# Optimization experiments

Measured on AMD Instinct MI355X. Metric: run time of the kernel, lower is better.

## Reference

```python
import jax, jax.numpy as jnp
import numpy as np

N = 100000          # n_nodes
E = 1600000         # n_edges (avg degree 16)
IN = 256            # in_dim
OUT = 16            # out_dim
SLOPE = 0.2         # leaky_relu negative slope
DROP = 0.5          # dropout rate


def _xavier(key, shape):
    fan_in, fan_out = shape
    std = (2.0 / (fan_in + fan_out)) ** 0.5
    return std * jax.random.normal(key, shape, jnp.float32)


def setup_inputs() -> dict:
    key = jax.random.key(0)
    ks = jax.random.split(key, 10)
    x = jax.random.normal(ks[0], (N, IN), jnp.float32)
    row = jax.random.randint(ks[1], (E,), 0, N, jnp.int32)
    col = jax.random.randint(ks[2], (E,), 0, N, jnp.int32)
    edge_w = jax.random.uniform(ks[3], (E,), jnp.float32)
    W1 = _xavier(ks[4], (IN, IN // 2)); b1 = jnp.zeros((IN // 2,), jnp.float32)
    W2 = _xavier(ks[5], (IN // 2, IN // 4)); b2 = jnp.zeros((IN // 4,), jnp.float32)
    W3 = _xavier(ks[6], (IN // 4, IN // 8)); b3 = jnp.zeros((IN // 8,), jnp.float32)
    W4 = _xavier(ks[7], (IN // 8, OUT)); b4 = jnp.zeros((OUT,), jnp.float32)
    # dropout mask (training-mode dropout made deterministic; pre-scaled by 1/(1-p))
    drop_mask = (jax.random.uniform(ks[8], (N, IN // 2)) > DROP).astype(jnp.float32) / (1.0 - DROP)
    return dict(x=x, row=row, col=col, edge_w=edge_w,
                W1=W1, b1=b1, W2=W2, b2=b2, W3=W3, b3=b3, W4=W4, b4=b4,
                drop_mask=drop_mask)


def reference(x, row, col, edge_w, W1, b1, W2, b2, W3, b3, W4, b4, drop_mask):
    def spmm(h):
        # out[i] = sum over edges (i <- j): w_ij * h[j]   (sparse adj @ h)
        return jax.ops.segment_sum(edge_w[:, None] * h[col], row, num_segments=N)

    lrelu = lambda v: jax.nn.leaky_relu(v, SLOPE)

    h = spmm(x @ W1) + b1          # gc1: [N, IN/2]
    h = lrelu(h) * drop_mask       # leaky_relu + dropout
    h = spmm(h @ W2) + b2          # gc2: [N, IN/4]
    h = lrelu(h)
    h = lrelu(h @ W3 + b3)         # clf hidden: [N, IN/8]
    return h @ W4 + b4             # logits: [N, OUT]
```

## Files before the change

kernel.cpp:

```cpp
#include <hip/hip_runtime.h>
#include <hip/hip_bf16.h>

#define N_NODES 100000
#define N_EDGES 1600000
#define SLOPE_ 0.2f
#define NBK 196
#define BCAP 9216
#define NCB 13
#define KEYS (512 * NCB)
#define BINBLK2 1000
#define CHUNK2 1600
#define PREPW 20
#define PMBLK 1563

typedef __attribute__((ext_vector_type(8))) short bf16x8;
typedef __attribute__((ext_vector_type(4))) float f32x4;

__device__ __forceinline__ short f2bf(float f) {
    __hip_bfloat16 h = __float2bfloat16(f);
    return *reinterpret_cast<short*>(&h);
}
__device__ __forceinline__ float bflo(unsigned u) { return __uint_as_float(u << 16); }
__device__ __forceinline__ float bfhi(unsigned u) { return __uint_as_float(u & 0xFFFF0000u); }
__device__ __forceinline__ float bf2f(short s) {
    return __uint_as_float(((unsigned)(unsigned short)s) << 16);
}


__global__ void countA_k(const int* __restrict__ row, int* __restrict__ counts,
                         const float* __restrict__ W1, const float* __restrict__ W2,
                         const float* __restrict__ mask,
                         short* __restrict__ Bp1, short* __restrict__ Bp2,
                         unsigned* __restrict__ mp) {
    int t = threadIdx.x;
    if (blockIdx.x < BINBLK2) {
        __shared__ int hist[NBK];
        for (int i = t; i < NBK; i += 256) hist[i] = 0;
        __syncthreads();
        int e0 = blockIdx.x * CHUNK2;
        for (int i = t; i < CHUNK2; i += 256)
            atomicAdd(&hist[row[e0 + i] >> 9], 1);
        __syncthreads();
        for (int i = t; i < NBK; i += 256)
            counts[(size_t)i * BINBLK2 + blockIdx.x] = hist[i];
        return;
    }
    int bi = blockIdx.x - BINBLK2;
    if (bi < PREPW) {
        int i = bi * 256 + t;
        if (i < 4096) {
            int ln = i & 15, nt = (i >> 4) & 7, g = (i >> 7) & 3, ks = i >> 9;
            int n = nt * 16 + ln, k0 = ks * 32 + g * 8;
            bf16x8 v;
#pragma unroll
            for (int j = 0; j < 8; j++) v[j] = f2bf(W1[(k0 + j) * 128 + n]);
            *(bf16x8*)(Bp1 + (size_t)i * 8) = v;
        } else if (i < 5120) {
            int c = i - 4096;
            int ln = c & 15, nt = (c >> 4) & 3, g = (c >> 6) & 3, ks = c >> 8;
            int n = nt * 16 + ln, k0 = ks * 32 + g * 8;
            bf16x8 v;
#pragma unroll
            for (int j = 0; j < 8; j++) v[j] = f2bf(W2[(k0 + j) * 64 + n]);
            *(bf16x8*)(Bp2 + (size_t)c * 8) = v;
        }
        return;
    }
    int pb = bi - PREPW;
    long fbase = (long)pb * 8192;
    int wv = t >> 6, lane = t & 63;
    const long FLIM = (long)N_NODES * 128;
    for (int it = 0; it < 32; ++it) {
        long f = fbase + it * 256 + wv * 64 + lane;
        float v = (f < FLIM) ? mask[f] : 0.f;
        unsigned long long bl = __ballot(v != 0.f);
        if (lane == 0) {
            long w = f >> 5;
            if (w < (long)N_NODES * 4)
                *(unsigned long long*)(mp + w) = bl;
        }
    }
}


__global__ void scanA_k(const int* __restrict__ counts, int* __restrict__ bases,
                        int* __restrict__ cur) {
    __shared__ int s[256];
    int b = blockIdx.x, t = threadIdx.x;
    const int* src = counts + (size_t)b * BINBLK2;
    int v[4];
    int loc = 0;
#pragma unroll
    for (int j = 0; j < 4; j++) {
        int idx = t * 4 + j;
        v[j] = (idx < BINBLK2) ? src[idx] : 0;
        loc += v[j];
    }
    s[t] = loc;
    __syncthreads();
    for (int off = 1; off < 256; off <<= 1) {
        int u = (t >= off) ? s[t - off] : 0;
        __syncthreads();
        s[t] += u;
        __syncthreads();
    }
    int run = s[t] - loc;
    int* dst = bases + (size_t)b * BINBLK2;
#pragma unroll
    for (int j = 0; j < 4; j++) {
        int idx = t * 4 + j;
        if (idx < BINBLK2) dst[idx] = run;
        run += v[j];
    }
    if (t == 255) cur[b] = min(s[255], BCAP);
}


__global__ void scatterA_k(const int* __restrict__ row, const int* __restrict__ col,
                           const float* __restrict__ ew, const int* __restrict__ bases,
                           int2* __restrict__ binned) {
    __shared__ int off[NBK];
    int t = threadIdx.x, blk = blockIdx.x;
    for (int i = t; i < NBK; i += 256) off[i] = bases[(size_t)i * BINBLK2 + blk];
    __syncthreads();
    int e0 = blk * CHUNK2;
    for (int i = t; i < CHUNK2; i += 256) {
        int e = e0 + i;
        int r = row[e], c = col[e];
        int b = r >> 9;
        int p = atomicAdd(&off[b], 1);
        if (p < BCAP)
            binned[(size_t)b * BCAP + p] =
                make_int2(((r & 511) << 17) | c, __float_as_int(ew[e]));
    }
}


__global__ void __launch_bounds__(512) passB_k(const int2* __restrict__ binned,
                                               const int* __restrict__ cur,
                                               unsigned* __restrict__ cw,
                                               int* __restrict__ row_ptr) {
    __shared__ int hist[KEYS];
    __shared__ int offs[KEYS];
    __shared__ int ssum[512];
    __shared__ int bexc[256];
    int t = threadIdx.x, b = blockIdx.x;
    const int2* src = binned + (size_t)b * BCAP;
    int cnt = cur[b];
    if (cnt > BCAP) cnt = BCAP;

    if (t < 256) bexc[t] = (t < NBK) ? min(cur[t], BCAP) : 0;
    __syncthreads();
    for (int off2 = 1; off2 < 256; off2 <<= 1) {
        int v = (t < 256 && t >= off2) ? bexc[t - off2] : 0;
        __syncthreads();
        if (t < 256) bexc[t] += v;
        __syncthreads();
    }
    int gbase = bexc[b] - cnt;

    for (int i = t; i < KEYS; i += 512) hist[i] = 0;
    __syncthreads();

    for (int i = t; i < cnt; i += 512) {
        int2 v = src[i];
        int c = v.x & 0x1FFFF, lr = v.x >> 17;
        atomicAdd(&hist[lr * NCB + (c >> 13)], 1);
    }
    __syncthreads();

    int loc[NCB];
    int tot = 0;
#pragma unroll
    for (int j = 0; j < NCB; j++) {
        loc[j] = tot;
        tot += hist[t * NCB + j];
    }
    ssum[t] = tot;
    __syncthreads();
    for (int off2 = 1; off2 < 512; off2 <<= 1) {
        int v = (t >= off2) ? ssum[t - off2] : 0;
        __syncthreads();
        ssum[t] += v;
        __syncthreads();
    }
    int base = ssum[t] - tot;
#pragma unroll
    for (int j = 0; j < NCB; j++) offs[t * NCB + j] = base + loc[j];

    int grow = b * 512 + t;
    if (grow <= N_NODES) row_ptr[grow] = gbase + base;
    __syncthreads();

    for (int i = t; i < cnt; i += 512) {
        int2 v = src[i];
        int c = v.x & 0x1FFFF, lr = v.x >> 17;
        int p = gbase + atomicAdd(&offs[lr * NCB + (c >> 13)], 1);
        unsigned wb = (unsigned)(unsigned short)f2bf(__int_as_float(v.y));
        cw[p] = ((unsigned)c << 15) | (wb & 0x7FFFu);
    }
}


template <int K, int COLS, bool ABF16>
__global__ __launch_bounds__(512) void gemm_p(const void* __restrict__ Ap,
                                              const short* __restrict__ Bp,
                                              short* __restrict__ out, int M) {
    constexpr int NT = COLS / 16;
    constexpr int NKS = K / 32;
    __shared__ short Bs[K * COLS];
    int t = threadIdx.x;
    for (int i = t; i < K * COLS / 8; i += 512)
        *(bf16x8*)(Bs + (size_t)i * 8) = *(const bf16x8*)(Bp + (size_t)i * 8);
    __syncthreads();

    int l = t & 63, wv = t >> 6;
    int ln = l & 15, g = l >> 4;
    int row0 = blockIdx.x * 256 + wv * 32;
    int r0 = row0 + ln, r1 = row0 + 16 + ln;
    int cr0 = min(r0, M - 1), cr1 = min(r1, M - 1);

    f32x4 acc[2][NT];
#pragma unroll
    for (int rf = 0; rf < 2; rf++)
#pragma unroll
        for (int nt = 0; nt < NT; nt++) acc[rf][nt] = (f32x4){0.f, 0.f, 0.f, 0.f};

#pragma unroll
    for (int ks = 0; ks < NKS; ks++) {
        int kk = ks * 32 + g * 8;
        bf16x8 a0, a1;
        if constexpr (ABF16) {
            a0 = *(const bf16x8*)((const short*)Ap + (size_t)cr0 * K + kk);
            a1 = *(const bf16x8*)((const short*)Ap + (size_t)cr1 * K + kk);
        } else {
            const float* p0 = (const float*)Ap + (size_t)cr0 * K + kk;
            const float* p1 = (const float*)Ap + (size_t)cr1 * K + kk;
            float4 u0 = *(const float4*)p0;
            float4 u1 = *(const float4*)(p0 + 4);
            float4 v0 = *(const float4*)p1;
            float4 v1 = *(const float4*)(p1 + 4);
            a0[0] = f2bf(u0.x); a0[1] = f2bf(u0.y); a0[2] = f2bf(u0.z); a0[3] = f2bf(u0.w);
            a0[4] = f2bf(u1.x); a0[5] = f2bf(u1.y); a0[6] = f2bf(u1.z); a0[7] = f2bf(u1.w);
            a1[0] = f2bf(v0.x); a1[1] = f2bf(v0.y); a1[2] = f2bf(v0.z); a1[3] = f2bf(v0.w);
            a1[4] = f2bf(v1.x); a1[5] = f2bf(v1.y); a1[6] = f2bf(v1.z); a1[7] = f2bf(v1.w);
        }
#pragma unroll
        for (int nt = 0; nt < NT; nt++) {
            bf16x8 b = *(const bf16x8*)(Bs + (size_t)((((ks * 4 + g) * NT + nt) * 16 + ln)) * 8);
            acc[0][nt] = __builtin_amdgcn_mfma_f32_16x16x32_bf16(a0, b, acc[0][nt], 0, 0, 0);
            acc[1][nt] = __builtin_amdgcn_mfma_f32_16x16x32_bf16(a1, b, acc[1][nt], 0, 0, 0);
        }
    }
#pragma unroll
    for (int rf = 0; rf < 2; rf++)
#pragma unroll
        for (int nt = 0; nt < NT; nt++)
#pragma unroll
            for (int r = 0; r < 4; r++) {
                int orow = row0 + rf * 16 + g * 4 + r;
                if (orow < M) out[(size_t)orow * COLS + nt * 16 + ln] = f2bf(acc[rf][nt][r]);
            }
}


template <int D, bool DROP>
__global__ void spmm_bf(const int* __restrict__ row_ptr, const unsigned* __restrict__ cwp,
                        const short* __restrict__ h,
                        const float* __restrict__ bias, const unsigned* __restrict__ maskp,
                        short* __restrict__ out, int n) {
    int bid = blockIdx.x;
    int sbid = (bid & 7) * 3125 + (bid >> 3);
    int wid = sbid * 4 + (int)(threadIdx.x >> 6);
    int lane = threadIdx.x & 63;
    if (wid >= n) return;
    int sp = __builtin_amdgcn_readfirstlane(row_ptr[wid]);
    int ep = __builtin_amdgcn_readfirstlane(row_ptr[wid + 1]);
    int cnt = ep - sp;
    const unsigned* pcw = cwp + sp;
    const unsigned* hb = (const unsigned*)h;
    float ax = 0.f, ay = 0.f;

    if (D == 128) {
        for (int jb = 0; jb < cnt; jb += 8) {
            unsigned u[8];
            float w[8];
#pragma unroll
            for (int p = 0; p < 8; p++) {
                int idx = jb + p;
                unsigned md = pcw[idx];
                md = (idx < cnt) ? md : 0u;
                int c = (int)(md >> 15);
                w[p] = __uint_as_float((md & 0x7FFFu) << 16);
                u[p] = hb[(size_t)c * 64 + lane];
            }
#pragma unroll
            for (int p = 0; p < 8; p++) {
                ax += w[p] * bflo(u[p]);
                ay += w[p] * bfhi(u[p]);
            }
        }
        float2 b = *(const float2*)(bias + 2 * lane);
        float ox = ax + b.x, oy = ay + b.y;
        ox = ox > 0.f ? ox : SLOPE_ * ox;
        oy = oy > 0.f ? oy : SLOPE_ * oy;
        if (DROP) {
            unsigned mw = maskp[(size_t)wid * 4 + (lane >> 4)];
            unsigned sh = (2 * lane) & 31;
            ox = ((mw >> sh) & 1u) ? 2.f * ox : 0.f;
            oy = ((mw >> (sh + 1)) & 1u) ? 2.f * oy : 0.f;
        }
        unsigned ov = (unsigned)(unsigned short)f2bf(ox) |
                      ((unsigned)(unsigned short)f2bf(oy) << 16);
        *(unsigned*)(out + (size_t)wid * 128 + 2 * lane) = ov;
    } else {
        int li = lane & 31;
        for (int jb = 0; jb < cnt; jb += 8) {
            unsigned u[4];
            float w[4];
#pragma unroll
            for (int p = 0; p < 4; p++) {
                int iA = jb + 2 * p, iB = iA + 1;
                unsigned mA = pcw[iA];
                mA = (iA < cnt) ? mA : 0u;
                unsigned mB = pcw[iB];
                mB = (iB < cnt) ? mB : 0u;
                unsigned md = (lane < 32) ? mA : mB;
                int c = (int)(md >> 15);
                w[p] = __uint_as_float((md & 0x7FFFu) << 16);
                u[p] = hb[(size_t)c * 32 + li];
            }
#pragma unroll
            for (int p = 0; p < 4; p++) {
                ax += w[p] * bflo(u[p]);
                ay += w[p] * bfhi(u[p]);
            }
        }
        ax += __shfl_xor(ax, 32);
        ay += __shfl_xor(ay, 32);
        float2 b = *(const float2*)(bias + li * 2);
        float ox = ax + b.x, oy = ay + b.y;
        ox = ox > 0.f ? ox : SLOPE_ * ox;
        oy = oy > 0.f ? oy : SLOPE_ * oy;
        unsigned ov = (unsigned)(unsigned short)f2bf(ox) |
                      ((unsigned)(unsigned short)f2bf(oy) << 16);
        if (lane < 32) *(unsigned*)(out + (size_t)wid * 64 + li * 2) = ov;
    }
}


__global__ void clf_k(const short* __restrict__ h, const float* __restrict__ W3,
                      const float* __restrict__ b3, const float* __restrict__ W4,
                      const float* __restrict__ b4, float* __restrict__ out) {
    __shared__ float W3s[64][32];
    __shared__ float W4s[32][16];
    __shared__ float b3s[32], b4s[16];
    __shared__ float hs[32][64];
    __shared__ float t4[32][33];
    int t = threadIdx.x;
    for (int l = t; l < 64 * 32; l += 256) W3s[l / 32][l % 32] = W3[l];
    for (int l = t; l < 32 * 16; l += 256) W4s[l / 16][l % 16] = W4[l];
    if (t < 32) b3s[t] = b3[t];
    if (t < 16) b4s[t] = b4[t];
    int row0 = blockIdx.x * 32;
    {
        bf16x8 v = *(const bf16x8*)(h + (size_t)row0 * 64 + t * 8);
        int r = t >> 3, c0 = (t & 7) << 3;
#pragma unroll
        for (int j = 0; j < 8; j++) hs[r][c0 + j] = bf2f(v[j]);
    }
    __syncthreads();
    for (int l = t; l < 1024; l += 256) {
        int r = l / 32, c = l % 32;
        float a = b3s[c];
#pragma unroll 8
        for (int k = 0; k < 64; k++) a += hs[r][k] * W3s[k][c];
        t4[r][c] = a > 0.f ? a : SLOPE_ * a;
    }
    __syncthreads();
    for (int l = t; l < 512; l += 256) {
        int r = l / 16, c = l % 16;
        float a = b4s[c];
#pragma unroll
        for (int k = 0; k < 32; k++) a += t4[r][k] * W4s[k][c];
        out[(size_t)(row0 + r) * 16 + c] = a;
    }
}


extern "C" void kernel_launch(void* const* d_in, const int* in_sizes, int n_in,
                              void* d_out, int out_size, void* d_ws, size_t ws_size,
                              hipStream_t stream) {
    const float* x = (const float*)d_in[0];
    const int* row = (const int*)d_in[1];
    const int* col = (const int*)d_in[2];
    const float* ew = (const float*)d_in[3];
    const float* W1 = (const float*)d_in[4];
    const float* b1 = (const float*)d_in[5];
    const float* W2 = (const float*)d_in[6];
    const float* b2 = (const float*)d_in[7];
    const float* W3 = (const float*)d_in[8];
    const float* b3 = (const float*)d_in[9];
    const float* W4 = (const float*)d_in[10];
    const float* b4 = (const float*)d_in[11];
    const float* mask = (const float*)d_in[12];
    float* out = (float*)d_out;

    const int N = N_NODES, E = N_EDGES;

    short* h0 = (short*)d_ws;
    short* h1 = h0 + (size_t)N * 128;
    short* h2 = h1 + (size_t)N * 128;
    short* h3 = h2 + (size_t)N * 64;
    short* Bp1 = h3 + (size_t)N * 64;
    short* Bp2 = Bp1 + 32768;
    int* row_ptr = (int*)(Bp2 + 8192);
    int* cur = row_ptr + N + 1;
    unsigned* mask_p = (unsigned*)(cur + NBK + 3);
    unsigned* cwp = mask_p + (size_t)N * 4;
    int* counts = (int*)(cwp + E + 16);
    int* bases = counts + NBK * BINBLK2;
    int2* binned = (int2*)h0;

    countA_k<<<BINBLK2 + PREPW + PMBLK, 256, 0, stream>>>(row, counts, W1, W2, mask,
                                                          Bp1, Bp2, mask_p);
    scanA_k<<<NBK, 256, 0, stream>>>(counts, bases, cur);
    scatterA_k<<<BINBLK2, 256, 0, stream>>>(row, col, ew, bases, binned);
    passB_k<<<NBK, 512, 0, stream>>>(binned, cur, cwp, row_ptr);

    gemm_p<256, 128, false><<<(N + 255) / 256, 512, 0, stream>>>(x, Bp1, h0, N);
    spmm_bf<128, true><<<25000, 256, 0, stream>>>(row_ptr, cwp, h0, b1, mask_p, h1, N);
    gemm_p<128, 64, true><<<(N + 255) / 256, 512, 0, stream>>>(h1, Bp2, h2, N);
    spmm_bf<64, false><<<25000, 256, 0, stream>>>(row_ptr, cwp, h2, b2, nullptr, h3, N);
    clf_k<<<N / 32, 256, 0, stream>>>(h3, W3, b3, W4, b4, out);
}
```

Baseline: 236.0 us.

## Fuse the second GEMM into the first SpMM and the classifier into the second SpMM

The first SpMM kernel now multiplies each node's dropped-out 128-wide row by W2 inside the wavefront, using shuffles and a W2 copy staged in LDS. This removes the h1 intermediate and the separate MFMA GEMM launch. The second SpMM now also computes the W3 and W4 classifier layers per node via shuffles, removing h3 and the clf kernel. The cost is a 16KB LDS load of W2 per block across 25000 blocks, and 64 scalar shuffle-FMA steps per node in place of the MFMA GEMM, which lowers occupancy and adds ALU and LDS work.

```diff
diff --git a/kernel.cpp b/kernel.cpp
--- a/kernel.cpp
+++ b/kernel.cpp
@@ -10,7 +10,7 @@
 #define KEYS (512 * NCB)
 #define BINBLK2 1000
 #define CHUNK2 1600
-#define PREPW 20
+#define PREPW 32
 #define PMBLK 1563
 
 typedef __attribute__((ext_vector_type(8))) short bf16x8;
@@ -25,12 +25,13 @@
 __device__ __forceinline__ float bf2f(short s) {
     return __uint_as_float(((unsigned)(unsigned short)s) << 16);
 }
+__device__ __forceinline__ float lrelu_(float v) { return v > 0.f ? v : SLOPE_ * v; }
 
 
 __global__ void countA_k(const int* __restrict__ row, int* __restrict__ counts,
                          const float* __restrict__ W1, const float* __restrict__ W2,
                          const float* __restrict__ mask,
-                         short* __restrict__ Bp1, short* __restrict__ Bp2,
+                         short* __restrict__ Bp1, unsigned* __restrict__ W2p,
                          unsigned* __restrict__ mp) {
     int t = threadIdx.x;
     if (blockIdx.x < BINBLK2) {
@@ -55,14 +56,12 @@
 #pragma unroll
             for (int j = 0; j < 8; j++) v[j] = f2bf(W1[(k0 + j) * 128 + n]);
             *(bf16x8*)(Bp1 + (size_t)i * 8) = v;
-        } else if (i < 5120) {
+        } else {
             int c = i - 4096;
-            int ln = c & 15, nt = (c >> 4) & 3, g = (c >> 6) & 3, ks = c >> 8;
-            int n = nt * 16 + ln, k0 = ks * 32 + g * 8;
-            bf16x8 v;
-#pragma unroll
-            for (int j = 0; j < 8; j++) v[j] = f2bf(W2[(k0 + j) * 64 + n]);
-            *(bf16x8*)(Bp2 + (size_t)c * 8) = v;
+            int k0 = c >> 6, j = c & 63;
+            unsigned lo = (unsigned)(unsigned short)f2bf(W2[(2 * k0) * 64 + j]);
+            unsigned hi = (unsigned)(unsigned short)f2bf(W2[(2 * k0 + 1) * 64 + j]);
+            W2p[c] = lo | (hi << 16);
         }
         return;
     }
@@ -264,15 +263,20 @@
 }
 
 
-template <int D, bool DROP>
-__global__ void spmm_bf(const int* __restrict__ row_ptr, const unsigned* __restrict__ cwp,
-                        const short* __restrict__ h,
-                        const float* __restrict__ bias, const unsigned* __restrict__ maskp,
-                        short* __restrict__ out, int n) {
+__global__ void spmm1g2_k(const int* __restrict__ row_ptr, const unsigned* __restrict__ cwp,
+                          const short* __restrict__ h,
+                          const float* __restrict__ b1, const unsigned* __restrict__ maskp,
+                          const unsigned* __restrict__ W2p,
+                          short* __restrict__ h2, int n) {
+    __shared__ unsigned W2s[4096];
+    int t = threadIdx.x;
+    for (int i = t; i < 4096; i += 256) W2s[i] = W2p[i];
+    __syncthreads();
+
     int bid = blockIdx.x;
     int sbid = (bid & 7) * 3125 + (bid >> 3);
-    int wid = sbid * 4 + (int)(threadIdx.x >> 6);
-    int lane = threadIdx.x & 63;
+    int wid = sbid * 4 + (t >> 6);
+    int lane = t & 63;
     if (wid >= n) return;
     int sp = __builtin_amdgcn_readfirstlane(row_ptr[wid]);
     int ep = __builtin_amdgcn_readfirstlane(row_ptr[wid + 1]);
@@ -281,110 +285,121 @@
     const unsigned* hb = (const unsigned*)h;
     float ax = 0.f, ay = 0.f;
 
-    if (D == 128) {
-        for (int jb = 0; jb < cnt; jb += 8) {
-            unsigned u[8];
-            float w[8];
-#pragma unroll
-            for (int p = 0; p < 8; p++) {
-                int idx = jb + p;
-                unsigned md = pcw[idx];
-                md = (idx < cnt) ? md : 0u;
-                int c = (int)(md >> 15);
-                w[p] = __uint_as_float((md & 0x7FFFu) << 16);
-                u[p] = hb[(size_t)c * 64 + lane];
-            }
-#pragma unroll
-            for (int p = 0; p < 8; p++) {
-                ax += w[p] * bflo(u[p]);
-                ay += w[p] * bfhi(u[p]);
-            }
-        }
-        float2 b = *(const float2*)(bias + 2 * lane);
-        float ox = ax + b.x, oy = ay + b.y;
-        ox = ox > 0.f ? ox : SLOPE_ * ox;
-        oy = oy > 0.f ? oy : SLOPE_ * oy;
-        if (DROP) {
-            unsigned mw = maskp[(size_t)wid * 4 + (lane >> 4)];
-            unsigned sh = (2 * lane) & 31;
-            ox = ((mw >> sh) & 1u) ? 2.f * ox : 0.f;
-            oy = ((mw >> (sh + 1)) & 1u) ? 2.f * oy : 0.f;
-        }
-        unsigned ov = (unsigned)(unsigned short)f2bf(ox) |
-                      ((unsigned)(unsigned short)f2bf(oy) << 16);
-        *(unsigned*)(out + (size_t)wid * 128 + 2 * lane) = ov;
-    } else {
-        int li = lane & 31;
-        for (int jb = 0; jb < cnt; jb += 8) {
-            unsigned u[4];
-            float w[4];
-#pragma unroll
-            for (int p = 0; p < 4; p++) {
-                int iA = jb + 2 * p, iB = iA + 1;
-                unsigned mA = pcw[iA];
-                mA = (iA < cnt) ? mA : 0u;
-                unsigned mB = pcw[iB];
-                mB = (iB < cnt) ? mB : 0u;
-                unsigned md = (lane < 32) ? mA : mB;
-                int c = (int)(md >> 15);
-                w[p] = __uint_as_float((md & 0x7FFFu) << 16);
-                u[p] = hb[(size_t)c * 32 + li];
-            }
-#pragma unroll
-            for (int p = 0; p < 4; p++) {
-                ax += w[p] * bflo(u[p]);
-                ay += w[p] * bfhi(u[p]);
-            }
-        }
-        ax += __shfl_xor(ax, 32);
-        ay += __shfl_xor(ay, 32);
-        float2 b = *(const float2*)(bias + li * 2);
-        float ox = ax + b.x, oy = ay + b.y;
-        ox = ox > 0.f ? ox : SLOPE_ * ox;
-        oy = oy > 0.f ? oy : SLOPE_ * oy;
-        unsigned ov = (unsigned)(unsigned short)f2bf(ox) |
-                      ((unsigned)(unsigned short)f2bf(oy) << 16);
-        if (lane < 32) *(unsigned*)(out + (size_t)wid * 64 + li * 2) = ov;
-    }
-}
-
-
-__global__ void clf_k(const short* __restrict__ h, const float* __restrict__ W3,
-                      const float* __restrict__ b3, const float* __restrict__ W4,
-                      const float* __restrict__ b4, float* __restrict__ out) {
-    __shared__ float W3s[64][32];
-    __shared__ float W4s[32][16];
+    for (int jb = 0; jb < cnt; jb += 8) {
+        unsigned u[8];
+        float w[8];
+#pragma unroll
+        for (int p = 0; p < 8; p++) {
+            int idx = jb + p;
+            unsigned md = pcw[idx];
+            md = (idx < cnt) ? md : 0u;
+            int c = (int)(md >> 15);
+            w[p] = __uint_as_float((md & 0x7FFFu) << 16);
+            u[p] = hb[(size_t)c * 64 + lane];
+        }
+#pragma unroll
+        for (int p = 0; p < 8; p++) {
+            ax += w[p] * bflo(u[p]);
+            ay += w[p] * bfhi(u[p]);
+        }
+    }
+    float2 b = *(const float2*)(b1 + 2 * lane);
+    float ox = lrelu_(ax + b.x), oy = lrelu_(ay + b.y);
+    unsigned mw = maskp[(size_t)wid * 4 + (lane >> 4)];
+    unsigned sh = (2 * lane) & 31;
+    ox = ((mw >> sh) & 1u) ? 2.f * ox : 0.f;
+    oy = ((mw >> (sh + 1)) & 1u) ? 2.f * oy : 0.f;
+
+    float o = 0.f;
+#pragma unroll 8
+    for (int k0 = 0; k0 < 64; k0++) {
+        float axk = __shfl(ox, k0);
+        float ayk = __shfl(oy, k0);
+        unsigned wv = W2s[k0 * 64 + lane];
+        o += axk * bflo(wv) + ayk * bfhi(wv);
+    }
+    *(unsigned short*)(h2 + (size_t)wid * 64 + lane) = (unsigned short)f2bf(o);
+}
+
+
+__global__ void spmm2c_k(const int* __restrict__ row_ptr, const unsigned* __restrict__ cwp,
+                         const short* __restrict__ h,
+                         const float* __restrict__ b2,
+                         const float* __restrict__ W3, const float* __restrict__ b3,
+                         const float* __restrict__ W4, const float* __restrict__ b4,
+                         float* __restrict__ out, int n) {
+    __shared__ float W3s[2048];
+    __shared__ float W4s[512];
     __shared__ float b3s[32], b4s[16];
-    __shared__ float hs[32][64];
-    __shared__ float t4[32][33];
     int t = threadIdx.x;
-    for (int l = t; l < 64 * 32; l += 256) W3s[l / 32][l % 32] = W3[l];
-    for (int l = t; l < 32 * 16; l += 256) W4s[l / 16][l % 16] = W4[l];
+    for (int i = t; i < 2048; i += 256) W3s[i] = W3[i];
+    for (int i = t; i < 512; i += 256) W4s[i] = W4[i];
     if (t < 32) b3s[t] = b3[t];
     if (t < 16) b4s[t] = b4[t];
-    int row0 = blockIdx.x * 32;
-    {
-        bf16x8 v = *(const bf16x8*)(h + (size_t)row0 * 64 + t * 8);
-        int r = t >> 3, c0 = (t & 7) << 3;
-#pragma unroll
-        for (int j = 0; j < 8; j++) hs[r][c0 + j] = bf2f(v[j]);
-    }
-    __syncthreads();
-    for (int l = t; l < 1024; l += 256) {
-        int r = l / 32, c = l % 32;
-        float a = b3s[c];
-#pragma unroll 8
-        for (int k = 0; k < 64; k++) a += hs[r][k] * W3s[k][c];
-        t4[r][c] = a > 0.f ? a : SLOPE_ * a;
-    }
-    __syncthreads();
-    for (int l = t; l < 512; l += 256) {
-        int r = l / 16, c = l % 16;
-        float a = b4s[c];
-#pragma unroll
-        for (int k = 0; k < 32; k++) a += t4[r][k] * W4s[k][c];
-        out[(size_t)(row0 + r) * 16 + c] = a;
-    }
+    __syncthreads();
+
+    int bid = blockIdx.x;
+    int sbid = (bid & 7) * 3125 + (bid >> 3);
+    int wid = sbid * 4 + (t >> 6);
+    int lane = t & 63;
+    if (wid >= n) return;
+    int sp = __builtin_amdgcn_readfirstlane(row_ptr[wid]);
+    int ep = __builtin_amdgcn_readfirstlane(row_ptr[wid + 1]);
+    int cnt = ep - sp;
+    const unsigned* pcw = cwp + sp;
+    const unsigned* hb = (const unsigned*)h;
+    int li = lane & 31;
+    float ax = 0.f, ay = 0.f;
+
+    for (int jb = 0; jb < cnt; jb += 8) {
+        unsigned u[4];
+        float w[4];
+#pragma unroll
+        for (int p = 0; p < 4; p++) {
+            int iA = jb + 2 * p, iB = iA + 1;
+            unsigned mA = pcw[iA];
+            mA = (iA < cnt) ? mA : 0u;
+            unsigned mB = pcw[iB];
+            mB = (iB < cnt) ? mB : 0u;
+            unsigned md = (lane < 32) ? mA : mB;
+            int c = (int)(md >> 15);
+            w[p] = __uint_as_float((md & 0x7FFFu) << 16);
+            u[p] = hb[(size_t)c * 32 + li];
+        }
+#pragma unroll
+        for (int p = 0; p < 4; p++) {
+            ax += w[p] * bflo(u[p]);
+            ay += w[p] * bfhi(u[p]);
+        }
+    }
+    ax += __shfl_xor(ax, 32);
+    ay += __shfl_xor(ay, 32);
+    float2 bb = *(const float2*)(b2 + 2 * li);
+    float sx = lrelu_(ax + bb.x);
+    float sy = lrelu_(ay + bb.y);
+
+    float p1 = 0.f;
+    int kbase = (lane >> 5) * 32;
+#pragma unroll
+    for (int i = 0; i < 32; i++) {
+        int k = kbase + i;
+        float sk = (i & 1) ? __shfl(sy, k >> 1) : __shfl(sx, k >> 1);
+        p1 += sk * W3s[k * 32 + li];
+    }
+    p1 += __shfl_xor(p1, 32);
+    float tj = lrelu_(p1 + b3s[li]);
+
+    float p2 = 0.f;
+    int c16 = lane & 15, kb2 = (lane >> 4) * 8;
+#pragma unroll
+    for (int i = 0; i < 8; i++) {
+        int k = kb2 + i;
+        float tk = __shfl(tj, k);
+        p2 += tk * W4s[k * 16 + c16];
+    }
+    p2 += __shfl_xor(p2, 16);
+    p2 += __shfl_xor(p2, 32);
+    if (lane < 16) out[(size_t)wid * 16 + lane] = p2 + b4s[lane];
 }
 
 
@@ -409,12 +424,10 @@
     const int N = N_NODES, E = N_EDGES;
 
     short* h0 = (short*)d_ws;
-    short* h1 = h0 + (size_t)N * 128;
-    short* h2 = h1 + (size_t)N * 128;
-    short* h3 = h2 + (size_t)N * 64;
-    short* Bp1 = h3 + (size_t)N * 64;
-    short* Bp2 = Bp1 + 32768;
-    int* row_ptr = (int*)(Bp2 + 8192);
+    short* h2 = h0 + (size_t)N * 128;
+    short* Bp1 = h2 + (size_t)N * 64;
+    unsigned* W2p = (unsigned*)(Bp1 + 32768);
+    int* row_ptr = (int*)(W2p + 4096);
     int* cur = row_ptr + N + 1;
     unsigned* mask_p = (unsigned*)(cur + NBK + 3);
     unsigned* cwp = mask_p + (size_t)N * 4;
@@ -423,14 +436,12 @@
     int2* binned = (int2*)h0;
 
     countA_k<<<BINBLK2 + PREPW + PMBLK, 256, 0, stream>>>(row, counts, W1, W2, mask,
-                                                          Bp1, Bp2, mask_p);
+                                                          Bp1, W2p, mask_p);
     scanA_k<<<NBK, 256, 0, stream>>>(counts, bases, cur);
     scatterA_k<<<BINBLK2, 256, 0, stream>>>(row, col, ew, bases, binned);
     passB_k<<<NBK, 512, 0, stream>>>(binned, cur, cwp, row_ptr);
 
     gemm_p<256, 128, false><<<(N + 255) / 256, 512, 0, stream>>>(x, Bp1, h0, N);
-    spmm_bf<128, true><<<25000, 256, 0, stream>>>(row_ptr, cwp, h0, b1, mask_p, h1, N);
-    gemm_p<128, 64, true><<<(N + 255) / 256, 512, 0, stream>>>(h1, Bp2, h2, N);
-    spmm_bf<64, false><<<25000, 256, 0, stream>>>(row_ptr, cwp, h2, b2, nullptr, h3, N);
-    clf_k<<<N / 32, 256, 0, stream>>>(h3, W3, b3, W4, b4, out);
-}
+    spmm1g2_k<<<25000, 256, 0, stream>>>(row_ptr, cwp, h0, b1, mask_p, W2p, h2, N);
+    spmm2c_k<<<25000, 256, 0, stream>>>(row_ptr, cwp, h2, b2, W3, b3, W4, b4, out, N);
+}
```

After: 337.6 us. 43.1% more time.

## Merge edge count, scan and scatter into one LDS-sorted binning kernel

Applied to the files above, without the earlier changes.

Replaces the three-kernel count/scan/scatter edge binning with one kernel. Each block builds a local histogram, reserves global slots per bin with atomics on a zeroed counter, sorts its chunk into bin order in shared memory, then writes it out in contiguous runs. This removes the counts/bases arrays, two launches and one extra pass over row. In exchange it uses far fewer, larger blocks with heavy LDS use, so there is less parallelism, and the order of edges within a bin now depends on how the atomics happen to run.

```diff
diff --git a/kernel.cpp b/kernel.cpp
--- a/kernel.cpp
+++ b/kernel.cpp
@@ -8,8 +8,8 @@
 #define BCAP 9216
 #define NCB 13
 #define KEYS (512 * NCB)
-#define BINBLK2 1000
-#define CHUNK2 1600
+#define BINBLK 256
+#define CHUNK 6250
 #define PREPW 20
 #define PMBLK 1563
 
@@ -27,27 +27,74 @@
 }
 
 
-__global__ void countA_k(const int* __restrict__ row, int* __restrict__ counts,
-                         const float* __restrict__ W1, const float* __restrict__ W2,
-                         const float* __restrict__ mask,
-                         short* __restrict__ Bp1, short* __restrict__ Bp2,
-                         unsigned* __restrict__ mp) {
+__global__ void zero_k(int* __restrict__ cur) {
+    if (threadIdx.x < NBK) cur[threadIdx.x] = 0;
+}
+
+
+__global__ __launch_bounds__(256) void bin_k(const int* __restrict__ row,
+                                             const int* __restrict__ col,
+                                             const float* __restrict__ ew,
+                                             int* __restrict__ cur,
+                                             int2* __restrict__ binned) {
+    __shared__ int hist[NBK];
+    __shared__ int lstart[NBK];
+    __shared__ int gbase[NBK];
+    __shared__ int off[NBK];
+    __shared__ int s[256];
+    __shared__ int2 sorted[CHUNK];
+    __shared__ int destg[CHUNK];
     int t = threadIdx.x;
-    if (blockIdx.x < BINBLK2) {
-        __shared__ int hist[NBK];
-        for (int i = t; i < NBK; i += 256) hist[i] = 0;
-        __syncthreads();
-        int e0 = blockIdx.x * CHUNK2;
-        for (int i = t; i < CHUNK2; i += 256)
-            atomicAdd(&hist[row[e0 + i] >> 9], 1);
-        __syncthreads();
-        for (int i = t; i < NBK; i += 256)
-            counts[(size_t)i * BINBLK2 + blockIdx.x] = hist[i];
-        return;
-    }
-    int bi = blockIdx.x - BINBLK2;
-    if (bi < PREPW) {
-        int i = bi * 256 + t;
+    int e0 = blockIdx.x * CHUNK;
+
+    for (int i = t; i < NBK; i += 256) hist[i] = 0;
+    __syncthreads();
+    for (int i = t; i < CHUNK; i += 256)
+        atomicAdd(&hist[row[e0 + i] >> 9], 1);
+    __syncthreads();
+
+    int h = (t < NBK) ? hist[t] : 0;
+    s[t] = h;
+    __syncthreads();
+    for (int o = 1; o < 256; o <<= 1) {
+        int v = (t >= o) ? s[t - o] : 0;
+        __syncthreads();
+        s[t] += v;
+        __syncthreads();
+    }
+    if (t < NBK) {
+        int ls = s[t] - h;
+        lstart[t] = ls;
+        off[t] = ls;
+        gbase[t] = atomicAdd(&cur[t], h);
+    }
+    __syncthreads();
+
+    for (int i = t; i < CHUNK; i += 256) {
+        int e = e0 + i;
+        int r = row[e], c = col[e];
+        int b = r >> 9;
+        int pos = atomicAdd(&off[b], 1);
+        sorted[pos] = make_int2(((r & 511) << 17) | c, __float_as_int(ew[e]));
+        int gidx = gbase[b] + (pos - lstart[b]);
+        destg[pos] = (gidx < BCAP) ? b * BCAP + gidx : -1;
+    }
+    __syncthreads();
+
+    for (int i = t; i < CHUNK; i += 256) {
+        int d = destg[i];
+        if (d >= 0) binned[d] = sorted[i];
+    }
+}
+
+
+__global__ void prep_pm_k(const float* __restrict__ W1, const float* __restrict__ W2,
+                          const float* __restrict__ mask,
+                          short* __restrict__ Bp1, short* __restrict__ Bp2,
+                          unsigned* __restrict__ mp) {
+    int t = threadIdx.x;
+    if (blockIdx.x < PREPW) {
+        int i = blockIdx.x * 256 + t;
         if (i < 4096) {
             int ln = i & 15, nt = (i >> 4) & 7, g = (i >> 7) & 3, ks = i >> 9;
             int n = nt * 16 + ln, k0 = ks * 32 + g * 8;
@@ -66,7 +113,7 @@
         }
         return;
     }
-    int pb = bi - PREPW;
+    int pb = blockIdx.x - PREPW;
     long fbase = (long)pb * 8192;
     int wv = t >> 6, lane = t & 63;
     const long FLIM = (long)N_NODES * 128;
@@ -79,59 +126,6 @@
             if (w < (long)N_NODES * 4)
                 *(unsigned long long*)(mp + w) = bl;
         }
-    }
-}
-
-
-__global__ void scanA_k(const int* __restrict__ counts, int* __restrict__ bases,
-                        int* __restrict__ cur) {
-    __shared__ int s[256];
-    int b = blockIdx.x, t = threadIdx.x;
-    const int* src = counts + (size_t)b * BINBLK2;
-    int v[4];
-    int loc = 0;
-#pragma unroll
-    for (int j = 0; j < 4; j++) {
-        int idx = t * 4 + j;
-        v[j] = (idx < BINBLK2) ? src[idx] : 0;
-        loc += v[j];
-    }
-    s[t] = loc;
-    __syncthreads();
-    for (int off = 1; off < 256; off <<= 1) {
-        int u = (t >= off) ? s[t - off] : 0;
-        __syncthreads();
-        s[t] += u;
-        __syncthreads();
-    }
-    int run = s[t] - loc;
-    int* dst = bases + (size_t)b * BINBLK2;
-#pragma unroll
-    for (int j = 0; j < 4; j++) {
-        int idx = t * 4 + j;
-        if (idx < BINBLK2) dst[idx] = run;
-        run += v[j];
-    }
-    if (t == 255) cur[b] = min(s[255], BCAP);
-}
-
-
-__global__ void scatterA_k(const int* __restrict__ row, const int* __restrict__ col,
-                           const float* __restrict__ ew, const int* __restrict__ bases,
-                           int2* __restrict__ binned) {
-    __shared__ int off[NBK];
-    int t = threadIdx.x, blk = blockIdx.x;
-    for (int i = t; i < NBK; i += 256) off[i] = bases[(size_t)i * BINBLK2 + blk];
-    __syncthreads();
-    int e0 = blk * CHUNK2;
-    for (int i = t; i < CHUNK2; i += 256) {
-        int e = e0 + i;
-        int r = row[e], c = col[e];
-        int b = r >> 9;
-        int p = atomicAdd(&off[b], 1);
-        if (p < BCAP)
-            binned[(size_t)b * BCAP + p] =
-                make_int2(((r & 511) << 17) | c, __float_as_int(ew[e]));
     }
 }
 
@@ -416,16 +410,13 @@
     short* Bp2 = Bp1 + 32768;
     int* row_ptr = (int*)(Bp2 + 8192);
     int* cur = row_ptr + N + 1;
-    unsigned* mask_p = (unsigned*)(cur + NBK + 3);
+    unsigned* mask_p = (unsigned*)(cur + NBK + 4);
     unsigned* cwp = mask_p + (size_t)N * 4;
-    int* counts = (int*)(cwp + E + 16);
-    int* bases = counts + NBK * BINBLK2;
     int2* binned = (int2*)h0;
 
-    countA_k<<<BINBLK2 + PREPW + PMBLK, 256, 0, stream>>>(row, counts, W1, W2, mask,
-                                                          Bp1, Bp2, mask_p);
-    scanA_k<<<NBK, 256, 0, stream>>>(counts, bases, cur);
-    scatterA_k<<<BINBLK2, 256, 0, stream>>>(row, col, ew, bases, binned);
+    zero_k<<<1, 256, 0, stream>>>(cur);
+    bin_k<<<BINBLK, 256, 0, stream>>>(row, col, ew, cur, binned);
+    prep_pm_k<<<PREPW + PMBLK, 256, 0, stream>>>(W1, W2, mask, Bp1, Bp2, mask_p);
     passB_k<<<NBK, 512, 0, stream>>>(binned, cur, cwp, row_ptr);
 
     gemm_p<256, 128, false><<<(N + 255) / 256, 512, 0, stream>>>(x, Bp1, h0, N);
```

After: 243.3 us. 3.1% more time.
